# Performance work log

Hardware: AMD Instinct MI355X
Metric: run time of the kernel (lower is better)

The kernel has to match this reference:

```python
import jax, jax.numpy as jnp
import numpy as np

K = 3            # kernel size (hard-coded in CANCRB_Down: conv 3x3, stride 1, pad 1)
PAD = 1
S_CLUSTERS = 32  # cluster_num
KMEANS_ITERS = 8 # fixed Lloyd iterations (jit-friendly stand-in for the repo's kmeans)


def extract_patches(x):
    # x [B,C,H,W] -> [B,C,9,H,W] (3x3 neighborhoods, zero pad 1) == F.unfold layout
    B, C, H, W = x.shape
    xp = jnp.pad(x, ((0, 0), (0, 0), (PAD, PAD), (PAD, PAD)))
    return jnp.stack([xp[:, :, i:i + H, j:j + W] for i in range(K) for j in range(K)], axis=2)


def setup_inputs() -> dict:
    key = jax.random.key(0)
    ks = jax.random.split(key, 6)
    B, C, H, W = 8, 64, 128, 128
    O = C
    return {
        "x": jax.random.normal(ks[0], (B, C, H, W), jnp.float32),
        # LAGConv2D params: per-pixel 3x3 kernel-attention conv + base weight
        "att_w": jax.random.normal(ks[1], (K * K, C, K, K), jnp.float32) * 0.05,
        "att_b": jnp.zeros((K * K,), jnp.float32),
        "w1": jax.random.normal(ks[2], (O, C, K, K), jnp.float32) * (1.0 / np.sqrt(C * K * K)),
        "b1": jnp.zeros((O,), jnp.float32),
        # CANConv params: kernel generator (centroid patch -> 3x3 spatial attention) + base weight
        "kg_w": jax.random.normal(ks[3], (K * K, C * K * K), jnp.float32) * 0.02,
        "kg_b": jnp.zeros((K * K,), jnp.float32),
        "w2": jax.random.normal(ks[4], (O, C, K * K), jnp.float32) * (1.0 / np.sqrt(C * K * K)),
        "b2": jnp.zeros((O,), jnp.float32),
    }


def _lagconv(x, att_w, att_b, w1, b1):
    # local adaptive gating conv: per-pixel k*k attention modulates the shared kernel
    att = jax.nn.sigmoid(
        jax.lax.conv_general_dilated(x, att_w, (1, 1), "SAME") + att_b[None, :, None, None]
    )  # [B,9,H,W]
    p = extract_patches(x)  # [B,C,9,H,W]
    O, C = w1.shape[0], w1.shape[1]
    y = jnp.einsum('bckhw,bkhw,ock->bohw', p, att, w1.reshape(O, C, K * K))
    return y + b1[None, :, None, None]


def _kmeans_assign(feat, cent):
    # feat [B,N,C], cent [B,S,C] -> idx [B,N]; drop the ||feat||^2 constant
    d = jnp.sum(cent * cent, axis=-1)[:, None, :] - 2.0 * jnp.einsum('bnc,bsc->bns', feat, cent)
    return jnp.argmin(d, axis=-1)


def _kmeans(feat, S):
    B, N, C = feat.shape
    cent = feat[:, ::max(N // S, 1), :][:, :S, :]  # deterministic evenly-spaced init
    for _ in range(KMEANS_ITERS):
        idx = _kmeans_assign(feat, cent)
        oh = jax.nn.one_hot(idx, S, dtype=feat.dtype)          # [B,N,S]
        cnt = jnp.clip(jnp.sum(oh, axis=1), 1.0)               # [B,S]
        cent = jnp.einsum('bns,bnc->bsc', oh, feat) / cnt[..., None]
    return _kmeans_assign(feat, cent)


def _canconv(x, kg_w, kg_b, w2, b2, S):
    B, C, H, W = x.shape
    N = H * W
    feat = x.reshape(B, C, N).transpose(0, 2, 1)               # per-pixel channel features
    idx = _kmeans(feat, S)                                     # [B,N] cluster assignment
    p = extract_patches(x).reshape(B, C * K * K, N).transpose(0, 2, 1)  # [B,N,C*9]
    oh = jax.nn.one_hot(idx, S, dtype=x.dtype)
    cnt = jnp.clip(jnp.sum(oh, axis=1), 1.0)
    cent_p = jnp.einsum('bns,bnp->bsp', oh, p) / cnt[..., None]         # cluster mean patches
    # per-cluster 3x3 spatial attention; scaled softmax keeps kernel magnitude ~ base weight
    att = jax.nn.softmax(cent_p @ kg_w.T + kg_b, axis=-1) * float(K * K)  # [B,S,9]
    a_pix = jnp.take_along_axis(att, idx[..., None], axis=1)             # gather: [B,N,9]
    pm = p.reshape(B, N, C, K * K) * a_pix[:, :, None, :]
    y = jnp.einsum('bnck,ock->bno', pm, w2) + b2                          # [B,N,O]
    return y.transpose(0, 2, 1).reshape(B, w2.shape[0], H, W), idx


def reference(x, att_w, att_b, w1, b1, kg_w, kg_b, w2, b2):
    # NOTE: original torch forward overwrites `res` -- conv1+relu output is discarded.
    # We compute it for FLOP parity but it does not affect the output (faithful to the bug).
    _dead = jax.nn.relu(_lagconv(x, att_w, att_b, w1, b1))
    res, idx = _canconv(x, kg_w, kg_b, w2, b2, S_CLUSTERS)
    out = x + res
    return out, idx
```

## Files before the change

kernel.cpp:

```cpp
#include <hip/hip_runtime.h>
#include <hip/hip_bf16.h>

#define Bn 8
#define Cn 64
#define Np 16384
#define Sc 32
#define On 64
#define Dd 576
#define KM_ITERS 8
#define KMB 64
#define KBLK 32

typedef float f32x4 __attribute__((ext_vector_type(4)));
typedef __bf16 bf16x8 __attribute__((ext_vector_type(8)));
typedef __bf16 bf16x4 __attribute__((ext_vector_type(4)));

__device__ __forceinline__ void split3(float v, __bf16& h, __bf16& m, __bf16& lo) {
    h = (__bf16)v;
    float r = v - (float)h;
    m = (__bf16)r;
    lo = (__bf16)(r - (float)m);
}

__device__ __forceinline__ void split2(float v, __bf16& h, __bf16& m) {
    h = (__bf16)v;
    m = (__bf16)(v - (float)h);
}

__global__ __launch_bounds__(256) void featbf2_k(const float* __restrict__ x,
                                                 __bf16* __restrict__ fh,
                                                 __bf16* __restrict__ fm) {
    __shared__ float tile[64][65];
    int b = blockIdx.y, n0 = blockIdx.x * 64, t = threadIdx.x;
    int j = t & 63, c0 = (t >> 6) * 16;
    #pragma unroll
    for (int cc = 0; cc < 16; ++cc)
        tile[c0 + cc][j] = x[((size_t)b * Cn + c0 + cc) * Np + n0 + j];
    __syncthreads();
    int n_loc = t & 63, cq = (t >> 6) * 16;
    bf16x8 vh[2], vm[2];
    #pragma unroll
    for (int g = 0; g < 2; ++g)
        #pragma unroll
        for (int u = 0; u < 8; ++u) {
            __bf16 h, m;
            split2(tile[cq + g * 8 + u][n_loc], h, m);
            vh[g][u] = h; vm[g][u] = m;
        }
    size_t base = ((size_t)b * Np + n0 + n_loc) * Cn + cq;
    *(bf16x8*)&fh[base] = vh[0]; *(bf16x8*)&fh[base + 8] = vh[1];
    *(bf16x8*)&fm[base] = vm[0]; *(bf16x8*)&fm[base + 8] = vm[1];
}

__global__ __launch_bounds__(64) void init_cent3_k(const float* __restrict__ x,
                                                   float* __restrict__ cent_f32,
                                                   __bf16* __restrict__ ch_,
                                                   __bf16* __restrict__ cm_,
                                                   float* __restrict__ cnorm) {
    int b = blockIdx.y, s = blockIdx.x, c = threadIdx.x;
    int n = s * (Np / Sc);
    float v = x[((size_t)b * Cn + c) * Np + n];
    int o = (b * Sc + s) * Cn + c;
    cent_f32[o] = v;
    __bf16 h, m; split2(v, h, m);
    ch_[o] = h; cm_[o] = m;
    float sq = v * v;
    #pragma unroll
    for (int off = 32; off >= 1; off >>= 1) sq += __shfl_down(sq, off);
    if (c == 0) cnorm[b * Sc + s] = sq;
}

__global__ __launch_bounds__(256) void w2prep_k(const float* __restrict__ w2,
                                                __bf16* __restrict__ w2kg) {
    int i = blockIdx.x * 256 + threadIdx.x;
    int k = i >> 12, rem = i & 4095, o = rem >> 6, c = rem & 63;
    w2kg[i] = (__bf16)w2[o * Dd + c * 9 + k];
}

__global__ __launch_bounds__(256, 3) void kmeans_fused3_k(
        const float* __restrict__ x,
        const __bf16* __restrict__ fh, const __bf16* __restrict__ fm,
        const float* __restrict__ cent_f32,
        const __bf16* __restrict__ ch_, const __bf16* __restrict__ cm_,
        const float* __restrict__ cnorm,
        int* __restrict__ idxg, float* __restrict__ gpart,
        float* __restrict__ out_idx, int do_update) {
    __shared__ __bf16 Bt_h[64][72];
    __shared__ __bf16 Bt_m[64][72];
    __shared__ __bf16 Bt_l[64][72];
    __shared__ __bf16 A_oh[32][72];
    __shared__ int idx_s[256];
    __shared__ int redint[4][32];
    __shared__ float centf_s[32][64];
    __shared__ float cnorm_s[32];
    int b = blockIdx.y, n0 = blockIdx.x * 256, t = threadIdx.x;
    int w = t >> 6, l = t & 63, arow = l & 15, kg = l >> 4;

    for (int i = t; i < Sc * Cn; i += 256) ((float*)centf_s)[i] = cent_f32[b * Sc * Cn + i];
    if (t < Sc) cnorm_s[t] = cnorm[b * Sc + t];

    bf16x8 cbh[2][2], cbm[2][2];
    #pragma unroll
    for (int st = 0; st < 2; ++st)
        #pragma unroll
        for (int kt = 0; kt < 2; ++kt) {
            size_t cb = (size_t)(b * Sc + st * 16 + arow) * Cn + kt * 32 + kg * 8;
            cbh[st][kt] = *(const bf16x8*)&ch_[cb];
            cbm[st][kt] = *(const bf16x8*)&cm_[cb];
        }
    float cn0 = cnorm[b * Sc + arow];
    float cn1 = cnorm[b * Sc + 16 + arow];

    f32x4 dacc[4][2];
    #pragma unroll
    for (int mt = 0; mt < 4; ++mt) {
        dacc[mt][0] = (f32x4){0.f, 0.f, 0.f, 0.f};
        dacc[mt][1] = (f32x4){0.f, 0.f, 0.f, 0.f};
    }
    #pragma unroll
    for (int mt = 0; mt < 4; ++mt) {
        size_t fb = ((size_t)b * Np + n0 + w * 64 + mt * 16 + arow) * Cn;
        bf16x8 ah[2], am2[2];
        #pragma unroll
        for (int kt = 0; kt < 2; ++kt) {
            ah[kt]  = *(const bf16x8*)&fh[fb + kt * 32 + kg * 8];
            am2[kt] = *(const bf16x8*)&fm[fb + kt * 32 + kg * 8];
        }
        #pragma unroll
        for (int st = 0; st < 2; ++st)
            #pragma unroll
            for (int kt = 0; kt < 2; ++kt) {
                dacc[mt][st] = __builtin_amdgcn_mfma_f32_16x16x32_bf16(ah[kt],  cbh[st][kt], dacc[mt][st], 0, 0, 0);
                dacc[mt][st] = __builtin_amdgcn_mfma_f32_16x16x32_bf16(ah[kt],  cbm[st][kt], dacc[mt][st], 0, 0, 0);
                dacc[mt][st] = __builtin_amdgcn_mfma_f32_16x16x32_bf16(am2[kt], cbh[st][kt], dacc[mt][st], 0, 0, 0);
                dacc[mt][st] = __builtin_amdgcn_mfma_f32_16x16x32_bf16(am2[kt], cbm[st][kt], dacc[mt][st], 0, 0, 0);
            }
    }
    __syncthreads();

    #pragma unroll
    for (int mt = 0; mt < 4; ++mt)
        #pragma unroll
        for (int r = 0; r < 4; ++r) {
            float dA = cn0 - 2.f * dacc[mt][0][r];
            float dB = cn1 - 2.f * dacc[mt][1][r];
            float d1, d2; int s1;
            if (dB < dA) { d1 = dB; s1 = arow + 16; d2 = dA; }
            else         { d1 = dA; s1 = arow;      d2 = dB; }
            #pragma unroll
            for (int mk = 1; mk < 16; mk <<= 1) {
                float d1o = __shfl_xor(d1, mk);
                int   s1o = __shfl_xor(s1, mk);
                float d2o = __shfl_xor(d2, mk);
                float big = fmaxf(d1, d1o);
                d2 = fminf(fminf(d2, d2o), big);
                if (d1o < d1 || (d1o == d1 && s1o < s1)) { d1 = d1o; s1 = s1o; }
            }
            int pix = w * 64 + mt * 16 + kg * 4 + r;
            bool writer = (arow == 0);
            if (writer) idx_s[pix] = s1;
            bool flag = writer && ((d2 - d1) < 0.02f);
            unsigned long long bal = __ballot(flag);
            while (bal) {
                int src = __ffsll(bal) - 1;
                bal &= bal - 1;
                int fp = w * 64 + mt * 16 + (src >> 4) * 4 + r;
                int n = n0 + fp;
                int s = l & 31, c0 = (l >> 5) * 32;
                float acc2 = 0.f;
                #pragma unroll 8
                for (int c = 0; c < 32; ++c)
                    acc2 = fmaf(x[((size_t)b * Cn + c0 + c) * Np + n], centf_s[s][c0 + c], acc2);
                acc2 += __shfl_xor(acc2, 32);
                float dd = cnorm_s[s] - 2.f * acc2;
                int ss = s;
                #pragma unroll
                for (int mk = 1; mk < 32; mk <<= 1) {
                    float ddo = __shfl_xor(dd, mk);
                    int   sso = __shfl_xor(ss, mk);
                    if (ddo < dd || (ddo == dd && sso < ss)) { dd = ddo; ss = sso; }
                }
                if (l == 0) idx_s[fp] = ss;
            }
        }
    __syncthreads();

    int best = idx_s[t];
    if (out_idx) {
        idxg[b * Np + n0 + t] = best;
        out_idx[b * Np + n0 + t] = (float)best;
    }
    if (!do_update) return;

    #pragma unroll 4
    for (int s = 0; s < Sc; ++s) {
        unsigned long long bal = __ballot(best == s);
        if (l == 0) redint[w][s] = __popcll(bal);
    }

    f32x4 uacc[2];
    uacc[0] = (f32x4){0.f, 0.f, 0.f, 0.f};
    uacc[1] = (f32x4){0.f, 0.f, 0.f, 0.f};
    for (int mc = 0; mc < 4; ++mc) {
        __syncthreads();
        {
            int c = t >> 2, mq = t & 3;
            const float* xp = &x[((size_t)b * Cn + c) * Np + n0 + mc * 64 + mq * 16];
            #pragma unroll
            for (int u = 0; u < 4; ++u) {
                f32x4 v = *(const f32x4*)&xp[u * 4];
                bf16x4 hv, mv, lv;
                #pragma unroll
                for (int e = 0; e < 4; ++e) {
                    __bf16 h, m, lo; split3(v[e], h, m, lo);
                    hv[e] = h; mv[e] = m; lv[e] = lo;
                }
                *(bf16x4*)&Bt_h[c][mq * 16 + u * 4] = hv;
                *(bf16x4*)&Bt_m[c][mq * 16 + u * 4] = mv;
                *(bf16x4*)&Bt_l[c][mq * 16 + u * 4] = lv;
            }
        }
        {
            int m = t & 63, sq = t >> 6;
            int bm = idx_s[mc * 64 + m];
            #pragma unroll
            for (int u = 0; u < 8; ++u)
                A_oh[sq * 8 + u][m] = (sq * 8 + u == bm) ? (__bf16)1.0f : (__bf16)0.0f;
        }
        __syncthreads();
        #pragma unroll
        for (int kh = 0; kh < 2; ++kh) {
            bf16x8 bh = *(const bf16x8*)&Bt_h[w * 16 + arow][kh * 32 + kg * 8];
            bf16x8 bm2 = *(const bf16x8*)&Bt_m[w * 16 + arow][kh * 32 + kg * 8];
            bf16x8 bl2 = *(const bf16x8*)&Bt_l[w * 16 + arow][kh * 32 + kg * 8];
            #pragma unroll
            for (int smt = 0; smt < 2; ++smt) {
                bf16x8 af = *(const bf16x8*)&A_oh[smt * 16 + arow][kh * 32 + kg * 8];
                uacc[smt] = __builtin_amdgcn_mfma_f32_16x16x32_bf16(af, bh,  uacc[smt], 0, 0, 0);
                uacc[smt] = __builtin_amdgcn_mfma_f32_16x16x32_bf16(af, bm2, uacc[smt], 0, 0, 0);
                uacc[smt] = __builtin_amdgcn_mfma_f32_16x16x32_bf16(af, bl2, uacc[smt], 0, 0, 0);
            }
        }
    }
    float* gp = &gpart[(size_t)(b * KMB + blockIdx.x) * (Sc * 65)];
    #pragma unroll
    for (int smt = 0; smt < 2; ++smt)
        #pragma unroll
        for (int r = 0; r < 4; ++r)
            gp[(smt * 16 + kg * 4 + r) * 65 + w * 16 + arow] = uacc[smt][r];
    if (t < Sc)
        gp[t * 65 + 64] = (float)(redint[0][t] + redint[1][t] + redint[2][t] + redint[3][t]);
}

__global__ __launch_bounds__(256) void update_reduce3_k(const float* __restrict__ gpart,
                                                        float* __restrict__ cent_f32,
                                                        __bf16* __restrict__ ch_,
                                                        __bf16* __restrict__ cm_,
                                                        float* __restrict__ cnorm) {
    __shared__ float psum[4][64];
    __shared__ float pcnt[4];
    int b = blockIdx.y, s = blockIdx.x, t = threadIdx.x;
    int w = t >> 6, c = t & 63;
    float sum = 0.f, cnt = 0.f;
    #pragma unroll 4
    for (int blk = w * 16; blk < w * 16 + 16; ++blk) {
        const float* g = &gpart[(size_t)(b * KMB + blk) * (Sc * 65) + s * 65];
        sum += g[c];
        if (c == 0) cnt += g[64];
    }
    psum[w][c] = sum;
    if (c == 0) pcnt[w] = cnt;
    __syncthreads();
    if (t < 64) {
        float m = psum[0][t] + psum[1][t] + psum[2][t] + psum[3][t];
        float ct = pcnt[0] + pcnt[1] + pcnt[2] + pcnt[3];
        float mean = m / fmaxf(ct, 1.f);
        int o = (b * Sc + s) * Cn + t;
        cent_f32[o] = mean;
        __bf16 h, mm; split2(mean, h, mm);
        ch_[o] = h; cm_[o] = mm;
        float sq = mean * mean;
        #pragma unroll
        for (int off = 32; off >= 1; off >>= 1) sq += __shfl_down(sq, off);
        if (t == 0) cnorm[b * Sc + s] = sq;
    }
}

__global__ __launch_bounds__(512) void centp_mfma_k(const float* __restrict__ x,
                                                    const int* __restrict__ idxg,
                                                    float* __restrict__ partialP) {
    __shared__ __bf16 Amat[288 * 56];
    __shared__ __bf16 Bt[64 * 56];
    int b = blockIdx.y, kb = blockIdx.x, t = threadIdx.x;
    int w = t >> 6, l = t & 63;
    int wm = w >> 2, wn = w & 3;
    int arow = l & 15, kg = l >> 4;
    f32x4 acc[9];
    #pragma unroll
    for (int j = 0; j < 9; ++j) acc[j] = (f32x4){0.f, 0.f, 0.f, 0.f};

    int m_base = kb * 512;
    for (int kt = 0; kt < 16; ++kt) {
        int m0 = m_base + kt * 32;
        #pragma unroll
        for (int j = 0; j < 9; ++j) {
            int i = t + 512 * j;
            int row = i >> 4, dc = i & 15;
            *(unsigned*)&Amat[row * 56 + dc * 2] = 0u;
        }
        {
            int c = t >> 3, k0 = (t & 7) * 4;
            f32x4 v = *(const f32x4*)&x[((size_t)b * Cn + c) * Np + m0 + k0];
            bf16x4 bv4;
            bv4[0] = (__bf16)v.x; bv4[1] = (__bf16)v.y;
            bv4[2] = (__bf16)v.z; bv4[3] = (__bf16)v.w;
            *(bf16x4*)&Bt[c * 56 + k0] = bv4;
        }
        __syncthreads();
        if (t < 288) {
            int m = t & 31, k = t >> 5;
            int mg = m0 + m, mh = mg >> 7, mw = mg & 127;
            int dh = k / 3 - 1, dw = k % 3 - 1;
            int nh = mh - dh, nw = mw - dw;
            if (((unsigned)nh < 128u) && ((unsigned)nw < 128u)) {
                int s = idxg[b * Np + (nh << 7) + nw];
                Amat[(s * 9 + k) * 56 + m] = (__bf16)1.0f;
            }
        }
        __syncthreads();
        bf16x8 bfrag = *(const bf16x8*)&Bt[(wn * 16 + arow) * 56 + kg * 8];
        #pragma unroll
        for (int j = 0; j < 9; ++j) {
            int mt = wm * 9 + j;
            bf16x8 afrag = *(const bf16x8*)&Amat[(mt * 16 + arow) * 56 + kg * 8];
            acc[j] = __builtin_amdgcn_mfma_f32_16x16x32_bf16(afrag, bfrag, acc[j], 0, 0, 0);
        }
        __syncthreads();
    }
    float* P = partialP + (size_t)(b * KBLK + kb) * 288 * 64;
    #pragma unroll
    for (int j = 0; j < 9; ++j) {
        int R0 = (wm * 9 + j) * 16 + kg * 4;
        int col = wn * 16 + arow;
        #pragma unroll
        for (int r = 0; r < 4; ++r) P[(size_t)(R0 + r) * 64 + col] = acc[j][r];
    }
}

__global__ __launch_bounds__(576) void centp_att2_k(const float* __restrict__ partialP,
                                                    const int* __restrict__ idxg,
                                                    const float* __restrict__ kg_w,
                                                    const float* __restrict__ kg_b,
                                                    float* __restrict__ attb) {
    __shared__ float cpm[9][64];
    __shared__ float logit[9];
    __shared__ int   redint[9];
    __shared__ float cnt_sh;
    int b = blockIdx.y, s = blockIdx.x, t = threadIdx.x;
    int k = t >> 6, c = t & 63;

    float sum = 0.f;
    for (int kb = 0; kb < KBLK; ++kb)
        sum += partialP[((size_t)(b * KBLK + kb) * 288 + s * 9 + k) * 64 + c];

    int cloc = 0;
    for (int i = t; i < Np; i += 576) cloc += (idxg[b * Np + i] == s);
    #pragma unroll
    for (int off = 32; off >= 1; off >>= 1) cloc += __shfl_down(cloc, off);
    if ((t & 63) == 0) redint[k] = cloc;
    __syncthreads();
    if (t == 0) {
        int c2 = 0;
        #pragma unroll
        for (int j = 0; j < 9; ++j) c2 += redint[j];
        cnt_sh = fmaxf((float)c2, 1.f);
    }
    __syncthreads();
    cpm[k][c] = sum / cnt_sh;
    __syncthreads();

    float pr = 0.f;
    #pragma unroll
    for (int u = 0; u < 9; ++u)
        pr = fmaf(cpm[u][c], kg_w[k * Dd + c * 9 + u], pr);
    #pragma unroll
    for (int off = 32; off >= 1; off >>= 1) pr += __shfl_down(pr, off);
    if ((t & 63) == 0) logit[k] = pr + kg_b[k];
    __syncthreads();
    if (t == 0) {
        float mx = logit[0];
        #pragma unroll
        for (int jj = 1; jj < 9; ++jj) mx = fmaxf(mx, logit[jj]);
        float e[9], sm = 0.f;
        #pragma unroll
        for (int jj = 0; jj < 9; ++jj) { e[jj] = expf(logit[jj] - mx); sm += e[jj]; }
        #pragma unroll
        for (int jj = 0; jj < 9; ++jj) attb[(b * Sc + s) * 9 + jj] = e[jj] / sm * 9.f;
    }
}

__global__ __launch_bounds__(512, 4) void final_out5_k(const float* __restrict__ x,
                                                       const __bf16* __restrict__ fh,
                                                       const int* __restrict__ idxg,
                                                       const float* __restrict__ attb,
                                                       const __bf16* __restrict__ w2kg,
                                                       const float* __restrict__ b2,
                                                       float* __restrict__ out) {
    __shared__ __align__(16) char smem[46080];
    __shared__ float apix_t[9][132];
    __shared__ float b2s[64];
    __bf16 (*w2l)[64][72] = (__bf16 (*)[64][72])smem;
    float (*trans)[132]   = (float (*)[132])smem;

    int b = blockIdx.y, hh = blockIdx.x, n0 = hh * 128, t = threadIdx.x;
    int w = t >> 6, l = t & 63, arow = l & 15, kg = l >> 4;

    if (t < 128) {
        int s = idxg[b * Np + n0 + t];
        const float* ap = attb + (b * Sc + s) * 9;
        #pragma unroll
        for (int k = 0; k < 9; ++k) apix_t[k][t] = ap[k];
    } else if (t < 192) {
        b2s[t - 128] = b2[t - 128];
    }
    for (int q = t; q < 2560; q += 512) {
        int kk = q >> 9, rem = q & 511, o = rem >> 3, c0 = (rem & 7) * 8;
        *(bf16x8*)&w2l[kk][o][c0] = *(const bf16x8*)&w2kg[(size_t)kk * 4096 + o * 64 + c0];
    }
    __syncthreads();

    int px = w * 16 + arow;
    f32x4 acc[4];
    #pragma unroll
    for (int nt = 0; nt < 4; ++nt) acc[nt] = (f32x4){0.f, 0.f, 0.f, 0.f};

    #define K_BODY(k, kk)                                                                  \
    {                                                                                      \
        const int dh = (k) / 3 - 1, dw = (k) % 3 - 1;                                      \
        int h2 = hh + dh, wc = px + dw;                                                    \
        bool valid = ((unsigned)h2 < 128u) && ((unsigned)wc < 128u);                       \
        const __bf16* fr = fh + (((size_t)b * Np + (h2 << 7) + wc) << 6);                  \
        bf16x8 av0 = (bf16x8)(__bf16)0.0f, av1 = (bf16x8)(__bf16)0.0f;                     \
        if (valid) {                                                                       \
            av0 = *(const bf16x8*)&fr[kg * 8];                                             \
            av1 = *(const bf16x8*)&fr[32 + kg * 8];                                        \
        }                                                                                  \
        f32x4 a4 = *(const f32x4*)&apix_t[k][w * 16 + kg * 4];                             \
        f32x4 acck[4];                                                                     \
        _Pragma("unroll")                                                                  \
        for (int nt = 0; nt < 4; ++nt) {                                                   \
            bf16x8 bv0 = *(const bf16x8*)&w2l[kk][nt * 16 + arow][kg * 8];                 \
            bf16x8 bv1 = *(const bf16x8*)&w2l[kk][nt * 16 + arow][32 + kg * 8];            \
            acck[nt] = __builtin_amdgcn_mfma_f32_16x16x32_bf16(av0, bv0,                   \
                           (f32x4){0.f, 0.f, 0.f, 0.f}, 0, 0, 0);                          \
            acck[nt] = __builtin_amdgcn_mfma_f32_16x16x32_bf16(av1, bv1, acck[nt], 0, 0, 0);\
        }                                                                                  \
        _Pragma("unroll")                                                                  \
        for (int nt = 0; nt < 4; ++nt)                                                     \
            _Pragma("unroll")                                                              \
            for (int r = 0; r < 4; ++r)                                                    \
                acc[nt][r] = fmaf(a4[r], acck[nt][r], acc[nt][r]);                         \
    }

    K_BODY(0, 0) K_BODY(1, 1) K_BODY(2, 2) K_BODY(3, 3) K_BODY(4, 4)
    __syncthreads();
    for (int q = t; q < 2048; q += 512) {
        int kk = q >> 9, rem = q & 511, o = rem >> 3, c0 = (rem & 7) * 8;
        *(bf16x8*)&w2l[kk][o][c0] = *(const bf16x8*)&w2kg[(size_t)(kk + 5) * 4096 + o * 64 + c0];
    }
    __syncthreads();
    K_BODY(5, 0) K_BODY(6, 1) K_BODY(7, 2) K_BODY(8, 3)
    #undef K_BODY

    __syncthreads();
    #pragma unroll
    for (int nt = 0; nt < 4; ++nt)
        #pragma unroll
        for (int r = 0; r < 4; ++r)
            trans[nt * 16 + arow][w * 16 + kg * 4 + r] = acc[nt][r];
    __syncthreads();
    for (int i = t; i < 8192; i += 512) {
        int o = i >> 7, p2 = i & 127;
        size_t gi = ((size_t)b * On + o) * Np + n0 + p2;
        out[gi] = x[gi] + trans[o][p2] + b2s[o];
    }
}

extern "C" void kernel_launch(void* const* d_in, const int* in_sizes, int n_in,
                              void* d_out, int out_size, void* d_ws, size_t ws_size,
                              hipStream_t stream) {
    (void)in_sizes; (void)n_in; (void)out_size; (void)ws_size;
    const float* x    = (const float*)d_in[0];
    const float* kg_w = (const float*)d_in[5];
    const float* kg_b = (const float*)d_in[6];
    const float* w2   = (const float*)d_in[7];
    const float* b2   = (const float*)d_in[8];
    float* out = (float*)d_out;

    char* p = (char*)d_ws;
    __bf16* fh      = (__bf16*)p; p += (size_t)Bn * Np * Cn * 2;
    __bf16* fm      = (__bf16*)p; p += (size_t)Bn * Np * Cn * 2;
    float*  cent_f32= (float*)p;  p += (size_t)Bn * Sc * Cn * 4;
    __bf16* ch_     = (__bf16*)p; p += (size_t)Bn * Sc * Cn * 2;
    __bf16* cm_     = (__bf16*)p; p += (size_t)Bn * Sc * Cn * 2;
    float*  cnorm   = (float*)p;  p += (size_t)Bn * Sc * 4;
    int*    idxg    = (int*)p;    p += (size_t)Bn * Np * 4;
    float*  gpart   = (float*)p;  p += (size_t)Bn * KMB * Sc * 65 * 4;
    float*  partialP= (float*)p;  p += (size_t)Bn * KBLK * 288 * 64 * 4;
    float*  attb    = (float*)p;  p += (size_t)Bn * Sc * 9 * 4;
    __bf16* w2kg    = (__bf16*)p; p += (size_t)9 * On * Cn * 2;

    featbf2_k<<<dim3(Np / 64, Bn), 256, 0, stream>>>(x, fh, fm);
    init_cent3_k<<<dim3(Sc, Bn), 64, 0, stream>>>(x, cent_f32, ch_, cm_, cnorm);
    w2prep_k<<<(On * Dd) / 256, 256, 0, stream>>>(w2, w2kg);

    for (int it = 0; it < KM_ITERS; ++it) {
        kmeans_fused3_k<<<dim3(KMB, Bn), 256, 0, stream>>>(
            x, fh, fm, cent_f32, ch_, cm_, cnorm, idxg, gpart, nullptr, 1);
        update_reduce3_k<<<dim3(Sc, Bn), 256, 0, stream>>>(gpart, cent_f32, ch_, cm_, cnorm);
    }
    kmeans_fused3_k<<<dim3(KMB, Bn), 256, 0, stream>>>(
        x, fh, fm, cent_f32, ch_, cm_, cnorm, idxg, gpart,
        out + (size_t)Bn * On * Np, 0);

    centp_mfma_k<<<dim3(KBLK, Bn), 512, 0, stream>>>(x, idxg, partialP);
    centp_att2_k<<<dim3(Sc, Bn), 576, 0, stream>>>(partialP, idxg, kg_w, kg_b, attb);

    final_out5_k<<<dim3(128, Bn), 512, 0, stream>>>(x, fh, idxg, attb, w2kg, b2, out);
}
```

Before: 401.7 us.

## Precompute channel-major bf16 split of x once and read it directly in kmeans/centp

The feature-prep kernel now also writes channel-major hi/mid/lo bf16 splits of x. The k-means update and the centroid-patch MFMA kernel load these as MFMA B fragments straight from global memory, instead of re-reading fp32 x and splitting it into shared memory on every iteration. The one-hot matrix is built once for all 256 pixels, which removes the per-chunk barriers. This costs extra workspace and write traffic up front, reuses the xm buffer for partialP, and trades LDS staging for uncoalesced-ish global fragment loads.

Measured after the change: 412.9 us. +2.8%, slower.

```diff
diff --git a/kernel.cpp b/kernel.cpp
--- a/kernel.cpp
+++ b/kernel.cpp
@@ -27,9 +27,12 @@
     m = (__bf16)(v - (float)h);
 }
 
-__global__ __launch_bounds__(256) void featbf2_k(const float* __restrict__ x,
+__global__ __launch_bounds__(256) void featbf4_k(const float* __restrict__ x,
                                                  __bf16* __restrict__ fh,
-                                                 __bf16* __restrict__ fm) {
+                                                 __bf16* __restrict__ fm,
+                                                 __bf16* __restrict__ xh,
+                                                 __bf16* __restrict__ xm,
+                                                 __bf16* __restrict__ xl) {
     __shared__ float tile[64][65];
     int b = blockIdx.y, n0 = blockIdx.x * 64, t = threadIdx.x;
     int j = t & 63, c0 = (t >> 6) * 16;
@@ -37,19 +40,38 @@
     for (int cc = 0; cc < 16; ++cc)
         tile[c0 + cc][j] = x[((size_t)b * Cn + c0 + cc) * Np + n0 + j];
     __syncthreads();
-    int n_loc = t & 63, cq = (t >> 6) * 16;
-    bf16x8 vh[2], vm[2];
-    #pragma unroll
-    for (int g = 0; g < 2; ++g)
-        #pragma unroll
-        for (int u = 0; u < 8; ++u) {
-            __bf16 h, m;
-            split2(tile[cq + g * 8 + u][n_loc], h, m);
-            vh[g][u] = h; vm[g][u] = m;
-        }
-    size_t base = ((size_t)b * Np + n0 + n_loc) * Cn + cq;
-    *(bf16x8*)&fh[base] = vh[0]; *(bf16x8*)&fh[base + 8] = vh[1];
-    *(bf16x8*)&fm[base] = vm[0]; *(bf16x8*)&fm[base + 8] = vm[1];
+
+    {
+        int n_loc = t & 63, cq = (t >> 6) * 16;
+        bf16x8 vh[2], vm[2];
+        #pragma unroll
+        for (int g = 0; g < 2; ++g)
+            #pragma unroll
+            for (int u = 0; u < 8; ++u) {
+                __bf16 h, m;
+                split2(tile[cq + g * 8 + u][n_loc], h, m);
+                vh[g][u] = h; vm[g][u] = m;
+            }
+        size_t base = ((size_t)b * Np + n0 + n_loc) * Cn + cq;
+        *(bf16x8*)&fh[base] = vh[0]; *(bf16x8*)&fh[base + 8] = vh[1];
+        *(bf16x8*)&fm[base] = vm[0]; *(bf16x8*)&fm[base + 8] = vm[1];
+    }
+    {
+        int c = t >> 2, jq = (t & 3) * 16;
+        bf16x8 hh[2], mm2[2], ll[2];
+        #pragma unroll
+        for (int g = 0; g < 2; ++g)
+            #pragma unroll
+            for (int u = 0; u < 8; ++u) {
+                __bf16 h, m, lo;
+                split3(tile[c][jq + g * 8 + u], h, m, lo);
+                hh[g][u] = h; mm2[g][u] = m; ll[g][u] = lo;
+            }
+        size_t cb = ((size_t)b * Cn + c) * Np + n0 + jq;
+        *(bf16x8*)&xh[cb] = hh[0]; *(bf16x8*)&xh[cb + 8] = hh[1];
+        *(bf16x8*)&xm[cb] = mm2[0]; *(bf16x8*)&xm[cb + 8] = mm2[1];
+        *(bf16x8*)&xl[cb] = ll[0]; *(bf16x8*)&xl[cb + 8] = ll[1];
+    }
 }
 
 __global__ __launch_bounds__(64) void init_cent3_k(const float* __restrict__ x,
@@ -77,18 +99,16 @@
     w2kg[i] = (__bf16)w2[o * Dd + c * 9 + k];
 }
 
-__global__ __launch_bounds__(256, 3) void kmeans_fused3_k(
+__global__ __launch_bounds__(256, 3) void kmeans_fused4_k(
         const float* __restrict__ x,
         const __bf16* __restrict__ fh, const __bf16* __restrict__ fm,
+        const __bf16* __restrict__ xh, const __bf16* __restrict__ xm, const __bf16* __restrict__ xl,
         const float* __restrict__ cent_f32,
         const __bf16* __restrict__ ch_, const __bf16* __restrict__ cm_,
         const float* __restrict__ cnorm,
         int* __restrict__ idxg, float* __restrict__ gpart,
         float* __restrict__ out_idx, int do_update) {
-    __shared__ __bf16 Bt_h[64][72];
-    __shared__ __bf16 Bt_m[64][72];
-    __shared__ __bf16 Bt_l[64][72];
-    __shared__ __bf16 A_oh[32][72];
+    __shared__ __bf16 A_oh[32][264];
     __shared__ int idx_s[256];
     __shared__ int redint[4][32];
     __shared__ float centf_s[32][64];
@@ -198,44 +218,25 @@
         if (l == 0) redint[w][s] = __popcll(bal);
     }
 
+    #pragma unroll
+    for (int s = 0; s < Sc; ++s)
+        A_oh[s][t] = (s == best) ? (__bf16)1.0f : (__bf16)0.0f;
+    __syncthreads();
+
     f32x4 uacc[2];
     uacc[0] = (f32x4){0.f, 0.f, 0.f, 0.f};
     uacc[1] = (f32x4){0.f, 0.f, 0.f, 0.f};
+    size_t xrow = ((size_t)b * Cn + (w * 16 + arow)) * Np + n0;
     for (int mc = 0; mc < 4; ++mc) {
-        __syncthreads();
-        {
-            int c = t >> 2, mq = t & 3;
-            const float* xp = &x[((size_t)b * Cn + c) * Np + n0 + mc * 64 + mq * 16];
-            #pragma unroll
-            for (int u = 0; u < 4; ++u) {
-                f32x4 v = *(const f32x4*)&xp[u * 4];
-                bf16x4 hv, mv, lv;
-                #pragma unroll
-                for (int e = 0; e < 4; ++e) {
-                    __bf16 h, m, lo; split3(v[e], h, m, lo);
-                    hv[e] = h; mv[e] = m; lv[e] = lo;
-                }
-                *(bf16x4*)&Bt_h[c][mq * 16 + u * 4] = hv;
-                *(bf16x4*)&Bt_m[c][mq * 16 + u * 4] = mv;
-                *(bf16x4*)&Bt_l[c][mq * 16 + u * 4] = lv;
-            }
-        }
-        {
-            int m = t & 63, sq = t >> 6;
-            int bm = idx_s[mc * 64 + m];
-            #pragma unroll
-            for (int u = 0; u < 8; ++u)
-                A_oh[sq * 8 + u][m] = (sq * 8 + u == bm) ? (__bf16)1.0f : (__bf16)0.0f;
-        }
-        __syncthreads();
         #pragma unroll
         for (int kh = 0; kh < 2; ++kh) {
-            bf16x8 bh = *(const bf16x8*)&Bt_h[w * 16 + arow][kh * 32 + kg * 8];
-            bf16x8 bm2 = *(const bf16x8*)&Bt_m[w * 16 + arow][kh * 32 + kg * 8];
-            bf16x8 bl2 = *(const bf16x8*)&Bt_l[w * 16 + arow][kh * 32 + kg * 8];
+            size_t off = xrow + mc * 64 + kh * 32 + kg * 8;
+            bf16x8 bh  = *(const bf16x8*)&xh[off];
+            bf16x8 bm2 = *(const bf16x8*)&xm[off];
+            bf16x8 bl2 = *(const bf16x8*)&xl[off];
             #pragma unroll
             for (int smt = 0; smt < 2; ++smt) {
-                bf16x8 af = *(const bf16x8*)&A_oh[smt * 16 + arow][kh * 32 + kg * 8];
+                bf16x8 af = *(const bf16x8*)&A_oh[smt * 16 + arow][mc * 64 + kh * 32 + kg * 8];
                 uacc[smt] = __builtin_amdgcn_mfma_f32_16x16x32_bf16(af, bh,  uacc[smt], 0, 0, 0);
                 uacc[smt] = __builtin_amdgcn_mfma_f32_16x16x32_bf16(af, bm2, uacc[smt], 0, 0, 0);
                 uacc[smt] = __builtin_amdgcn_mfma_f32_16x16x32_bf16(af, bl2, uacc[smt], 0, 0, 0);
@@ -286,11 +287,10 @@
     }
 }
 
-__global__ __launch_bounds__(512) void centp_mfma_k(const float* __restrict__ x,
-                                                    const int* __restrict__ idxg,
-                                                    float* __restrict__ partialP) {
+__global__ __launch_bounds__(512) void centp_mfma2_k(const __bf16* __restrict__ xh,
+                                                     const int* __restrict__ idxg,
+                                                     float* __restrict__ partialP) {
     __shared__ __bf16 Amat[288 * 56];
-    __shared__ __bf16 Bt[64 * 56];
     int b = blockIdx.y, kb = blockIdx.x, t = threadIdx.x;
     int w = t >> 6, l = t & 63;
     int wm = w >> 2, wn = w & 3;
@@ -300,6 +300,7 @@
     for (int j = 0; j < 9; ++j) acc[j] = (f32x4){0.f, 0.f, 0.f, 0.f};
 
     int m_base = kb * 512;
+    size_t xrow = ((size_t)b * Cn + wn * 16 + arow) * Np;
     for (int kt = 0; kt < 16; ++kt) {
         int m0 = m_base + kt * 32;
         #pragma unroll
@@ -307,14 +308,6 @@
             int i = t + 512 * j;
             int row = i >> 4, dc = i & 15;
             *(unsigned*)&Amat[row * 56 + dc * 2] = 0u;
-        }
-        {
-            int c = t >> 3, k0 = (t & 7) * 4;
-            f32x4 v = *(const f32x4*)&x[((size_t)b * Cn + c) * Np + m0 + k0];
-            bf16x4 bv4;
-            bv4[0] = (__bf16)v.x; bv4[1] = (__bf16)v.y;
-            bv4[2] = (__bf16)v.z; bv4[3] = (__bf16)v.w;
-            *(bf16x4*)&Bt[c * 56 + k0] = bv4;
         }
         __syncthreads();
         if (t < 288) {
@@ -328,7 +321,7 @@
             }
         }
         __syncthreads();
-        bf16x8 bfrag = *(const bf16x8*)&Bt[(wn * 16 + arow) * 56 + kg * 8];
+        bf16x8 bfrag = *(const bf16x8*)&xh[xrow + m0 + kg * 8];
         #pragma unroll
         for (int j = 0; j < 9; ++j) {
             int mt = wm * 9 + j;
@@ -500,30 +493,33 @@
     char* p = (char*)d_ws;
     __bf16* fh      = (__bf16*)p; p += (size_t)Bn * Np * Cn * 2;
     __bf16* fm      = (__bf16*)p; p += (size_t)Bn * Np * Cn * 2;
+    __bf16* xh      = (__bf16*)p; p += (size_t)Bn * Np * Cn * 2;
+    __bf16* xm      = (__bf16*)p; p += (size_t)Bn * Np * Cn * 2;
+    __bf16* xl      = (__bf16*)p; p += (size_t)Bn * Np * Cn * 2;
     float*  cent_f32= (float*)p;  p += (size_t)Bn * Sc * Cn * 4;
     __bf16* ch_     = (__bf16*)p; p += (size_t)Bn * Sc * Cn * 2;
     __bf16* cm_     = (__bf16*)p; p += (size_t)Bn * Sc * Cn * 2;
     float*  cnorm   = (float*)p;  p += (size_t)Bn * Sc * 4;
     int*    idxg    = (int*)p;    p += (size_t)Bn * Np * 4;
     float*  gpart   = (float*)p;  p += (size_t)Bn * KMB * Sc * 65 * 4;
-    float*  partialP= (float*)p;  p += (size_t)Bn * KBLK * 288 * 64 * 4;
     float*  attb    = (float*)p;  p += (size_t)Bn * Sc * 9 * 4;
     __bf16* w2kg    = (__bf16*)p; p += (size_t)9 * On * Cn * 2;
-
-    featbf2_k<<<dim3(Np / 64, Bn), 256, 0, stream>>>(x, fh, fm);
+    float*  partialP = (float*)xm;
+
+    featbf4_k<<<dim3(Np / 64, Bn), 256, 0, stream>>>(x, fh, fm, xh, xm, xl);
     init_cent3_k<<<dim3(Sc, Bn), 64, 0, stream>>>(x, cent_f32, ch_, cm_, cnorm);
     w2prep_k<<<(On * Dd) / 256, 256, 0, stream>>>(w2, w2kg);
 
     for (int it = 0; it < KM_ITERS; ++it) {
-        kmeans_fused3_k<<<dim3(KMB, Bn), 256, 0, stream>>>(
-            x, fh, fm, cent_f32, ch_, cm_, cnorm, idxg, gpart, nullptr, 1);
+        kmeans_fused4_k<<<dim3(KMB, Bn), 256, 0, stream>>>(
+            x, fh, fm, xh, xm, xl, cent_f32, ch_, cm_, cnorm, idxg, gpart, nullptr, 1);
         update_reduce3_k<<<dim3(Sc, Bn), 256, 0, stream>>>(gpart, cent_f32, ch_, cm_, cnorm);
     }
-    kmeans_fused3_k<<<dim3(KMB, Bn), 256, 0, stream>>>(
-        x, fh, fm, cent_f32, ch_, cm_, cnorm, idxg, gpart,
+    kmeans_fused4_k<<<dim3(KMB, Bn), 256, 0, stream>>>(
+        x, fh, fm, xh, xm, xl, cent_f32, ch_, cm_, cnorm, idxg, gpart,
         out + (size_t)Bn * On * Np, 0);
 
-    centp_mfma_k<<<dim3(KBLK, Bn), 512, 0, stream>>>(x, idxg, partialP);
+    centp_mfma2_k<<<dim3(KBLK, Bn), 512, 0, stream>>>(xh, idxg, partialP);
     centp_att2_k<<<dim3(Sc, Bn), 576, 0, stream>>>(partialP, idxg, kg_w, kg_b, attb);
 
     final_out5_k<<<dim3(128, Bn), 512, 0, stream>>>(x, fh, idxg, attb, w2kg, b2, out);
```
